# Optimization experiments

Measured on AMD Instinct MI355X. Metric: run time of the kernel, lower is better.

The kernel has to match this reference:

```python
import jax, jax.numpy as jnp
import numpy as np

B, C, H, W = 8, 64, 256, 512
FOV = np.pi / 4.0
KH = KW = 3


def _sphere_indices(H, W, fov):
    """Nearest-neighbor gather indices for a 3x3 spherical (gnomonic) kernel
    of angular extent `fov` on an equirectangular grid. Returns int32 [H, W, 9]."""
    taps = [(p, q) for p in (-1, 0, 1) for q in (-1, 0, 1)]
    theta = (0.5 - (np.arange(H) + 0.5) / H) * np.pi            # latitude per row [H]
    phi = ((np.arange(W) + 0.5) / W - 0.5) * 2.0 * np.pi        # longitude per col [W]
    r = np.tan(fov / 2.0)                                       # tangent-plane half extent
    gi_l, gj_l = [], []
    for (p, q) in taps:
        y_t, x_t = p * r, q * r
        rho = np.hypot(x_t, y_t)
        if rho == 0.0:
            lat = theta
            lon_off = np.zeros_like(theta)
        else:
            nu = np.arctan(rho)
            lat = np.arcsin(np.clip(np.cos(nu) * np.sin(theta)
                                    + y_t * np.sin(nu) * np.cos(theta) / rho, -1.0, 1.0))
            lon_off = np.arctan2(x_t * np.sin(nu),
                                 rho * np.cos(theta) * np.cos(nu)
                                 - y_t * np.sin(theta) * np.sin(nu))
        lon = phi[None, :] + lon_off[:, None]                   # [H, W]
        gi = np.clip(np.round((0.5 - lat / np.pi) * H - 0.5), 0, H - 1).astype(np.int32)
        gi = np.broadcast_to(gi[:, None], (H, W)).copy()
        gj = (np.round((lon / (2.0 * np.pi) + 0.5) * W - 0.5).astype(np.int64) % W).astype(np.int32)
        gi_l.append(gi)
        gj_l.append(gj)
    return np.stack(gi_l, axis=-1), np.stack(gj_l, axis=-1)    # [H, W, 9] each


def setup_inputs() -> dict:
    key = jax.random.key(0)
    k1, k2 = jax.random.split(key)
    feature = jax.random.normal(k1, (B, C, H, W), dtype=jnp.float32)
    weight = jax.random.normal(k2, (1, C, KH, KW), dtype=jnp.float32) * 0.05
    gi, gj = _sphere_indices(H, W, FOV)
    return {"feature": feature, "weight": weight,
            "gi": jnp.asarray(gi), "gj": jnp.asarray(gj)}


def reference(feature, weight, gi, gj):
    # SphericalConv: gather-based 3x3 conv over spherical sampling grid, stride 1, no bias.
    O, Cc, kh, kw = weight.shape
    wflat = weight.reshape(O, Cc, kh * kw)                      # [O, C, 9]
    Bb = feature.shape[0]
    Hh, Ww = gi.shape[0], gi.shape[1]
    out = jnp.zeros((Bb, O, Hh, Ww), feature.dtype)
    for k in range(kh * kw):                                    # fixed 9-tap loop
        xk = feature[:, :, gi[:, :, k], gj[:, :, k]]            # gather -> [B, C, H, W]
        out = out + jnp.einsum('bchw,oc->bohw', xk, wflat[:, :, k])
    # nn.Upsample(scale_factor=2) default nearest
    return jnp.repeat(jnp.repeat(out, 2, axis=2), 2, axis=3)
```

## Files before the change

### kernel.cpp

```cpp
#include <hip/hip_runtime.h>

#define Bn   8
#define Cn   64
#define Hn   256
#define Wn   512
#define HWn  (Hn * Wn)
#define TAPS 9

typedef float vfloat2 __attribute__((ext_vector_type(2)));

__global__ __launch_bounds__(256) void pass1_chandot(
    const float* __restrict__ feat, const float* __restrict__ wt,
    float* __restrict__ D)
{
    const int p = blockIdx.x * 256 + threadIdx.x;

    float acc[TAPS][Bn];
#pragma unroll
    for (int k = 0; k < TAPS; ++k)
#pragma unroll
        for (int b = 0; b < Bn; ++b) acc[k][b] = 0.f;

    float buf[2][4][Bn];

#pragma unroll
    for (int ci = 0; ci < 4; ++ci)
#pragma unroll
        for (int b = 0; b < Bn; ++b)
            buf[0][ci][b] = __builtin_nontemporal_load(
                feat + (size_t)(b * Cn + ci) * HWn + p);

#pragma unroll
    for (int g = 0; g < 16; ++g) {
        const int cur = g & 1, nxt = cur ^ 1;
        if (g < 15) {
            const int c0 = (g + 1) * 4;
#pragma unroll
            for (int ci = 0; ci < 4; ++ci)
#pragma unroll
                for (int b = 0; b < Bn; ++b)
                    buf[nxt][ci][b] = __builtin_nontemporal_load(
                        feat + (size_t)(b * Cn + c0 + ci) * HWn + p);
        }
#pragma unroll
        for (int ci = 0; ci < 4; ++ci) {
            const int c = g * 4 + ci;
#pragma unroll
            for (int k = 0; k < TAPS; ++k) {
                const float wv = wt[c * TAPS + k];
#pragma unroll
                for (int b = 0; b < Bn; ++b)
                    acc[k][b] = fmaf(buf[cur][ci][b], wv, acc[k][b]);
            }
        }
    }

#pragma unroll
    for (int k = 0; k < TAPS; ++k) {
        float4* dst = (float4*)(D + ((size_t)k * HWn + p) * Bn);
        dst[0] = make_float4(acc[k][0], acc[k][1], acc[k][2], acc[k][3]);
        dst[1] = make_float4(acc[k][4], acc[k][5], acc[k][6], acc[k][7]);
    }
}

__global__ __launch_bounds__(256) void pass2_gather(
    const float* __restrict__ D, const int* __restrict__ gi,
    const int* __restrict__ gj, float* __restrict__ out)
{
    __shared__ int loff[256 * TAPS];
    const int tid   = threadIdx.x;
    const int p0    = blockIdx.x * 256;
    const int gbase = p0 * TAPS;

#pragma unroll
    for (int i = tid; i < 256 * TAPS; i += 256)
        loff[i] = gi[gbase + i] * Wn + gj[gbase + i];
    __syncthreads();

    const int p = p0 + tid;
    const int w = p & (Wn - 1);
    const int h = p >> 9;

    float a[Bn];
#pragma unroll
    for (int b = 0; b < Bn; ++b) a[b] = 0.f;

#pragma unroll
    for (int k = 0; k < TAPS; ++k) {
        const int off = loff[tid * TAPS + k];
        const float4* d = (const float4*)(D + ((size_t)k * HWn + off) * Bn);
        float4 d0 = d[0], d1 = d[1];
        a[0] += d0.x; a[1] += d0.y; a[2] += d0.z; a[3] += d0.w;
        a[4] += d1.x; a[5] += d1.y; a[6] += d1.z; a[7] += d1.w;
    }

#pragma unroll
    for (int b = 0; b < Bn; ++b) {
        vfloat2 vv = {a[b], a[b]};
        size_t o = ((size_t)b * (2 * Hn) + 2 * h) * (size_t)(2 * Wn) + 2 * w;
        __builtin_nontemporal_store(vv, (vfloat2*)(out + o));
        __builtin_nontemporal_store(vv, (vfloat2*)(out + o + 2 * Wn));
    }
}

__global__ __launch_bounds__(256) void direct_kernel(
    const float* __restrict__ feat, const float* __restrict__ wt,
    const int* __restrict__ gi, const int* __restrict__ gj,
    float* __restrict__ out)
{
    int p = blockIdx.x * blockDim.x + threadIdx.x;
    int w = p & (Wn - 1);
    int h = (p >> 9) & (Hn - 1);
    int b = p >> 17;

    int iidx = ((h << 9) | w) * TAPS;
    int off[TAPS];
#pragma unroll
    for (int k = 0; k < TAPS; ++k)
        off[k] = gi[iidx + k] * Wn + gj[iidx + k];

    float acc = 0.f;
    for (int c = 0; c < Cn; ++c) {
        const float* fc = feat + ((size_t)b * Cn + c) * HWn;
#pragma unroll
        for (int k = 0; k < TAPS; ++k)
            acc = fmaf(fc[off[k]], wt[c * TAPS + k], acc);
    }

    float2 v = make_float2(acc, acc);
    size_t o0 = ((size_t)b * (2 * Hn) + 2 * h) * (size_t)(2 * Wn) + 2 * w;
    *(float2*)(out + o0)          = v;
    *(float2*)(out + o0 + 2 * Wn) = v;
}

extern "C" void kernel_launch(void* const* d_in, const int* in_sizes, int n_in,
                              void* d_out, int out_size, void* d_ws, size_t ws_size,
                              hipStream_t stream) {
    const float* feat = (const float*)d_in[0];
    const float* wt   = (const float*)d_in[1];
    const int*   gi   = (const int*)d_in[2];
    const int*   gj   = (const int*)d_in[3];
    float*       out  = (float*)d_out;

    const size_t bytesD = (size_t)TAPS * HWn * Bn * sizeof(float);

    if (ws_size >= bytesD) {
        float* D = (float*)d_ws;
        pass1_chandot<<<HWn / 256, 256, 0, stream>>>(feat, wt, D);
        pass2_gather <<<HWn / 256, 256, 0, stream>>>(D, gi, gj, out);
    } else {
        direct_kernel<<<(Bn * HWn) / 256, 256, 0, stream>>>(feat, wt, gi, gj, out);
    }
}
```

Measured before the change: 365.4 us.

## Split pass1 batch into two halves to double grid and raise occupancy

Pass1 now handles four batch images per block instead of eight and launches twice as many blocks, so each thread carries fewer accumulators and buffers, and launch bounds ask for four blocks per SIMD. The intermediate tensor is stored as two half-batch planes per tap. Pass2 issues all eighteen float4 gathers up front before summing, to expose more memory-level parallelism. The cost is that each pass2 gather is split into two separate 16-byte loads from different planes, and pass1 reloads the weights once per half.

```diff
diff --git a/kernel.cpp b/kernel.cpp
--- a/kernel.cpp
+++ b/kernel.cpp
@@ -6,29 +6,33 @@
 #define Wn   512
 #define HWn  (Hn * Wn)
 #define TAPS 9
+#define BH   4
 
 typedef float vfloat2 __attribute__((ext_vector_type(2)));
 
-__global__ __launch_bounds__(256) void pass1_chandot(
+__global__ __launch_bounds__(256, 4) void pass1_chandot(
     const float* __restrict__ feat, const float* __restrict__ wt,
     float* __restrict__ D)
 {
-    const int p = blockIdx.x * 256 + threadIdx.x;
+    const int strip = blockIdx.x & 511;
+    const int half  = blockIdx.x >> 9;
+    const int p     = strip * 256 + (int)threadIdx.x;
+    const float* fbase = feat + (size_t)half * BH * Cn * HWn + p;
 
-    float acc[TAPS][Bn];
+    float acc[TAPS][BH];
 #pragma unroll
     for (int k = 0; k < TAPS; ++k)
 #pragma unroll
-        for (int b = 0; b < Bn; ++b) acc[k][b] = 0.f;
+        for (int b = 0; b < BH; ++b) acc[k][b] = 0.f;
 
-    float buf[2][4][Bn];
+    float buf[2][4][BH];
 
 #pragma unroll
     for (int ci = 0; ci < 4; ++ci)
 #pragma unroll
-        for (int b = 0; b < Bn; ++b)
+        for (int b = 0; b < BH; ++b)
             buf[0][ci][b] = __builtin_nontemporal_load(
-                feat + (size_t)(b * Cn + ci) * HWn + p);
+                fbase + (size_t)(b * Cn + ci) * HWn);
 
 #pragma unroll
     for (int g = 0; g < 16; ++g) {
@@ -38,9 +42,9 @@
 #pragma unroll
             for (int ci = 0; ci < 4; ++ci)
 #pragma unroll
-                for (int b = 0; b < Bn; ++b)
+                for (int b = 0; b < BH; ++b)
                     buf[nxt][ci][b] = __builtin_nontemporal_load(
-                        feat + (size_t)(b * Cn + c0 + ci) * HWn + p);
+                        fbase + (size_t)(b * Cn + c0 + ci) * HWn);
         }
 #pragma unroll
         for (int ci = 0; ci < 4; ++ci) {
@@ -49,7 +53,7 @@
             for (int k = 0; k < TAPS; ++k) {
                 const float wv = wt[c * TAPS + k];
 #pragma unroll
-                for (int b = 0; b < Bn; ++b)
+                for (int b = 0; b < BH; ++b)
                     acc[k][b] = fmaf(buf[cur][ci][b], wv, acc[k][b]);
             }
         }
@@ -57,9 +61,8 @@
 
 #pragma unroll
     for (int k = 0; k < TAPS; ++k) {
-        float4* dst = (float4*)(D + ((size_t)k * HWn + p) * Bn);
-        dst[0] = make_float4(acc[k][0], acc[k][1], acc[k][2], acc[k][3]);
-        dst[1] = make_float4(acc[k][4], acc[k][5], acc[k][6], acc[k][7]);
+        float4* dst = (float4*)(D + ((size_t)(k * 2 + half) * HWn + p) * BH);
+        *dst = make_float4(acc[k][0], acc[k][1], acc[k][2], acc[k][3]);
     }
 }
 
@@ -81,17 +84,24 @@
     const int w = p & (Wn - 1);
     const int h = p >> 9;
 
+    int off[TAPS];
+#pragma unroll
+    for (int k = 0; k < TAPS; ++k) off[k] = loff[tid * TAPS + k];
+
+    float4 x0[TAPS], x1[TAPS];
+#pragma unroll
+    for (int k = 0; k < TAPS; ++k) {
+        x0[k] = *(const float4*)(D + ((size_t)(2 * k)     * HWn + off[k]) * BH);
+        x1[k] = *(const float4*)(D + ((size_t)(2 * k + 1) * HWn + off[k]) * BH);
+    }
+
     float a[Bn];
 #pragma unroll
     for (int b = 0; b < Bn; ++b) a[b] = 0.f;
-
 #pragma unroll
     for (int k = 0; k < TAPS; ++k) {
-        const int off = loff[tid * TAPS + k];
-        const float4* d = (const float4*)(D + ((size_t)k * HWn + off) * Bn);
-        float4 d0 = d[0], d1 = d[1];
-        a[0] += d0.x; a[1] += d0.y; a[2] += d0.z; a[3] += d0.w;
-        a[4] += d1.x; a[5] += d1.y; a[6] += d1.z; a[7] += d1.w;
+        a[0] += x0[k].x; a[1] += x0[k].y; a[2] += x0[k].z; a[3] += x0[k].w;
+        a[4] += x1[k].x; a[5] += x1[k].y; a[6] += x1[k].z; a[7] += x1[k].w;
     }
 
 #pragma unroll
@@ -142,11 +152,11 @@
     const int*   gj   = (const int*)d_in[3];
     float*       out  = (float*)d_out;
 
-    const size_t bytesD = (size_t)TAPS * HWn * Bn * sizeof(float);
+    const size_t bytesD = (size_t)TAPS * 2 * HWn * BH * sizeof(float);
 
     if (ws_size >= bytesD) {
         float* D = (float*)d_ws;
-        pass1_chandot<<<HWn / 256, 256, 0, stream>>>(feat, wt, D);
+        pass1_chandot<<<2 * (HWn / 256), 256, 0, stream>>>(feat, wt, D);
         pass2_gather <<<HWn / 256, 256, 0, stream>>>(D, gi, gj, out);
     } else {
         direct_kernel<<<(Bn * HWn) / 256, 256, 0, stream>>>(feat, wt, gi, gj, out);
```

Measured after the change: 364.6 us (median of 2 runs). About the same (-0.2%).
